# Optimization experiments

Measured on AMD Instinct MI355X. Metric: run time of the kernel, lower is better.

## Reference

```python
import jax, jax.numpy as jnp
import numpy as np

B, N, E, C = 2, 10000, 150000, 256
EPS = 1e-5  # torch BatchNorm1d default eps


def _bn(x, gamma, beta):
    # BatchNorm1d in training mode: biased batch statistics over the row dim.
    m = x.mean(axis=0)
    v = x.var(axis=0)
    return (x - m) * jax.lax.rsqrt(v + EPS) * gamma + beta


def setup_inputs() -> dict:
    key = jax.random.key(0)
    ks = jax.random.split(key, 6)
    xyz = jax.random.normal(ks[0], (B, N, 3), jnp.float32)
    features = jax.random.normal(ks[1], (B, C, N), jnp.float32)
    edges = jax.random.randint(ks[2], (B, 2, E), 0, N, jnp.int32)
    W_e = jax.random.normal(ks[3], (C + 3, C), jnp.float32) * 0.02
    b_e = jnp.zeros((C,), jnp.float32)
    g_e = jnp.ones((C,), jnp.float32)
    beta_e = jnp.zeros((C,), jnp.float32)
    W_u = jax.random.normal(ks[4], (C, C), jnp.float32) * 0.02
    b_u = jnp.zeros((C,), jnp.float32)
    g_u = jnp.ones((C,), jnp.float32)
    beta_u = jnp.zeros((C,), jnp.float32)
    return {"xyz": xyz, "features": features, "edges": edges,
            "W_e": W_e, "b_e": b_e, "g_e": g_e, "beta_e": beta_e,
            "W_u": W_u, "b_u": b_u, "g_u": g_u, "beta_u": beta_u}


def reference(xyz, features, edges, W_e, b_e, g_e, beta_e, W_u, b_u, g_u, beta_u):
    vf = jnp.transpose(features, (0, 2, 1))        # [B, N, C]
    ed = jnp.transpose(edges, (0, 2, 1))           # [B, E, 2]
    src, dst = ed[..., 0], ed[..., 1]              # [B, E]
    gather = jax.vmap(lambda v, i: v[i])
    s_feat = gather(vf, src)                       # [B, E, C]
    s_xyz = gather(xyz, src)                       # [B, E, 3]
    d_xyz = gather(xyz, dst)                       # [B, E, 3]
    ef = jnp.concatenate([s_feat, s_xyz - d_xyz], axis=-1).reshape(-1, C + 3)
    h = _bn(jax.nn.relu(ef @ W_e + b_e), g_e, beta_e).reshape(B, E, C)
    # scatter-max by destination vertex
    agg = jax.vmap(lambda f, i: jax.ops.segment_max(f, i, num_segments=N))(h, dst)
    agg = jnp.where(jnp.isfinite(agg), agg, 0.0)   # empty segments -> 0 (torch_scatter fill)
    u = _bn(jax.nn.relu(agg.reshape(-1, C) @ W_u + b_u), g_u, beta_u).reshape(B, N, C)
    out = u + vf                                   # residual
    return jnp.transpose(out, (0, 2, 1))           # [B, C, N]
```

## Files before the change

### kernel.cpp

```cpp
#include <hip/hip_runtime.h>

#define B_ 2
#define N_ 10000
#define E_ 150000
#define C_ 256
#define M_EDGE (B_*E_)
#define M_NODE (B_*N_)
#define ED_CAP (M_EDGE + 3*M_NODE + 64)
#define NW_ 4096
#define SPAN_CAP 256
#define EPS_ 1e-5f

typedef unsigned short u16;
typedef unsigned int   u32;
typedef unsigned long long u64;
typedef __attribute__((ext_vector_type(8))) __bf16 bf16x8;
typedef __attribute__((ext_vector_type(4))) float  f32x4;
typedef _Float16 h2 __attribute__((ext_vector_type(2)));

__device__ __forceinline__ u16 f2bf(float x) {
  union { float f; u32 u; } v; v.f = x;
  u32 r = v.u + 0x7FFFu + ((v.u >> 16) & 1u);
  return (u16)(r >> 16);
}
__device__ __forceinline__ float bf2f(u16 x) {
  union { u32 u; float f; } v; v.u = ((u32)x) << 16; return v.f;
}
__device__ __forceinline__ u16 f2h(float x) {
  _Float16 h = (_Float16)x;
  union { _Float16 h; u16 u; } v; v.h = h; return v.u;
}
__device__ __forceinline__ float h2f(u32 bits) {
  union { u16 u; _Float16 h; } v; v.u = (u16)bits; return (float)v.h;
}
__device__ __forceinline__ h2 u2h2(u32 x) {
  union { u32 u; h2 h; } v; v.u = x; return v.h;
}
__device__ __forceinline__ u32 h22u(h2 x) {
  union { h2 h; u32 u; } v; v.h = x; return v.u;
}

__device__ __forceinline__ void async16(void* lds, const void* g) {
  __builtin_amdgcn_global_load_lds(
      (const __attribute__((address_space(1))) void*)g,
      (__attribute__((address_space(3))) void*)lds, 16, 0, 0);
}

__device__ __forceinline__ u32 zload(const u16* zp, u32 si) {
  u32 r;
  u64 a = (u64)(zp + ((size_t)si << 8));
  asm volatile("global_load_dword %0, %1, off" : "=v"(r) : "v"(a) : "memory");
  return r;
}

__global__ void k_transpose_feat(const float* __restrict__ f, u16* __restrict__ vf,
                                 int* __restrict__ counts, float* __restrict__ stats) {
  __shared__ float tile[32][33];
  int tx = threadIdx.x & 31, ty = threadIdx.x >> 5;
  int b = blockIdx.z, c0 = blockIdx.y * 32, n0 = blockIdx.x * 32;
  if (blockIdx.y == 0 && blockIdx.z == 0) {
    int i = blockIdx.x * 256 + threadIdx.x;
    if (i < M_NODE) counts[i] = 0;
    if (i < 1024) stats[i] = 0.f;
  }
  #pragma unroll
  for (int i = 0; i < 4; i++) {
    int c = c0 + ty + i*8, n = n0 + tx;
    tile[ty + i*8][tx] = (n < N_) ? f[((size_t)(b*C_ + c))*N_ + n] : 0.f;
  }
  __syncthreads();
  #pragma unroll
  for (int i = 0; i < 4; i++) {
    int n = n0 + ty + i*8, c = c0 + tx;
    if (n < N_) vf[((size_t)(b*N_ + n))*C_ + c] = f2bf(tile[tx][ty + i*8]);
  }
}

__global__ void k_transpose_w(const float* __restrict__ We, const float* __restrict__ Wu,
                              u16* __restrict__ WeT, u16* __restrict__ WuT) {
  __shared__ float tile[32][33];
  const float* src = blockIdx.z ? Wu : We;
  u16* dst = blockIdx.z ? WuT : WeT;
  int tx = threadIdx.x & 31, ty = threadIdx.x >> 5;
  int r0 = blockIdx.y * 32, c0 = blockIdx.x * 32;
  #pragma unroll
  for (int i = 0; i < 4; i++)
    tile[ty + i*8][tx] = src[(size_t)(r0 + ty + i*8)*C_ + c0 + tx];
  __syncthreads();
  #pragma unroll
  for (int i = 0; i < 4; i++)
    dst[(size_t)(c0 + ty + i*8)*C_ + r0 + tx] = f2bf(tile[tx][ty + i*8]);
}

__global__ void k_hist(const int* __restrict__ edges, int* __restrict__ counts) {
  int i = blockIdx.x * 256 + threadIdx.x;
  if (i >= M_EDGE) return;
  int b = (i >= E_) ? 1 : 0;
  int e = i - b * E_;
  int d = edges[(size_t)(b*2 + 1)*E_ + e];
  atomicAdd(&counts[b*N_ + d], 1);
}

__global__ __launch_bounds__(1024)
void k_scan(const int* __restrict__ counts, int* __restrict__ offs, int* __restrict__ cursor) {
  __shared__ int wsum[16];
  int t = threadIdx.x;
  int lane = t & 63, wv = t >> 6;
  int base = t * 20;
  int vals[20];
  if (t < 1000) {
    #pragma unroll
    for (int j = 0; j < 5; j++)
      *(int4*)&vals[j*4] = *(const int4*)&counts[base + j*4];
  } else {
    #pragma unroll
    for (int i = 0; i < 20; i++) vals[i] = 0;
  }
  int local[20];
  int tot = 0;
  #pragma unroll
  for (int i = 0; i < 20; i++) {
    int pv = (vals[i] + 3) & ~3;
    local[i] = tot; tot += pv;
  }
  int inc = tot;
  #pragma unroll
  for (int d = 1; d < 64; d <<= 1) {
    int v = __shfl_up(inc, d, 64);
    if (lane >= d) inc += v;
  }
  if (lane == 63) wsum[wv] = inc;
  __syncthreads();
  if (t < 16) {
    int v = wsum[t];
    int inc2 = v;
    #pragma unroll
    for (int d = 1; d < 16; d <<= 1) {
      int x = __shfl_up(inc2, d, 16);
      if (t >= d) inc2 += x;
    }
    wsum[t] = inc2 - v;
  }
  __syncthreads();
  int excl = wsum[wv] + inc - tot;
  if (t < 1000) {
    #pragma unroll
    for (int j = 0; j < 5; j++) {
      int4 o;
      o.x = excl + local[j*4 + 0];
      o.y = excl + local[j*4 + 1];
      o.z = excl + local[j*4 + 2];
      o.w = excl + local[j*4 + 3];
      *(int4*)&offs[base + j*4]   = o;
      *(int4*)&cursor[base + j*4] = o;
    }
  }
  if (t == 1023) offs[M_NODE] = excl + tot;
}

__global__ void k_scatter(const int* __restrict__ edges, const float* __restrict__ xyz,
                          int* __restrict__ cursor, uint2* __restrict__ ed) {
  int i = blockIdx.x * 256 + threadIdx.x;
  if (i >= M_EDGE) return;
  int b = (i >= E_) ? 1 : 0;
  int e = i - b * E_;
  int s = edges[(size_t)(b*2 + 0)*E_ + e];
  int d = edges[(size_t)(b*2 + 1)*E_ + e];
  const float* ps = xyz + ((size_t)(b*N_ + s))*3;
  const float* pd = xyz + ((size_t)(b*N_ + d))*3;
  int pos = atomicAdd(&cursor[b*N_ + d], 1);
  u32 rx = (u32)f2h(ps[0]-pd[0]) | ((u32)f2h(ps[1]-pd[1]) << 16);
  u32 ry = (u32)f2h(ps[2]-pd[2]) | ((u32)(b*N_ + s) << 16);
  ed[pos] = make_uint2(rx, ry);
}

__global__ void k_pad(const int* __restrict__ offs, const int* __restrict__ counts,
                      uint2* __restrict__ ed, u32* __restrict__ nodeInfo,
                      int* __restrict__ waveStart) {
  int i = blockIdx.x * 256 + threadIdx.x;
  const int T = offs[M_NODE];
  const int SPW = (T + NW_ - 1) / NW_;
  if (i < M_NODE) {
    int s = offs[i], e = offs[i+1];
    int cnt = counts[i];
    if (cnt > 0) {
      int pad = e - (s + cnt);
      if (pad) {
        uint2 f = ed[s];
        for (int k = 0; k < pad; k++) ed[s + cnt + k] = f;
      }
    }
    nodeInfo[i] = ((u32)e << 10) | (u32)cnt;
    int lo = (i == 0) ? 0 : offs[i-1] + 1;
    int wlo = (lo + SPW - 1) / SPW;
    int whi = offs[i] / SPW;
    for (int w = wlo; w <= whi && w <= NW_; w++) waveStart[w] = i;
  }
  if (i == M_NODE) {
    nodeInfo[M_NODE]   = ((u32)T << 10);
    nodeInfo[M_NODE+1] = ((u32)T << 10);
    int lo = offs[M_NODE-1] + 1;
    int wlo = (lo + SPW - 1) / SPW;
    if (wlo < 0) wlo = 0;
    for (int w = wlo; w <= NW_; w++) waveStart[w] = M_NODE;
  }
  int pos = T + i;
  if (pos < ED_CAP) ed[pos] = make_uint2(0u, 0u);
}

__global__ __launch_bounds__(256)
void k_zgemm(const u16* __restrict__ A, const u16* __restrict__ WeT,
             const float* __restrict__ be, u16* __restrict__ zh)
{
  __shared__ __align__(16) u16 As[128*32];
  __shared__ __align__(16) u16 Bs[128*32];
  const int t  = threadIdx.x;
  const int n0 = blockIdx.x * 128;
  const int mb = blockIdx.y * 128;

  int r0 = mb + (t >> 2);      if (r0 >= M_NODE) r0 = 0;
  int r1 = mb + 64 + (t >> 2); if (r1 >= M_NODE) r1 = 0;
  const int ak = (((t & 3) ^ ((t >> 3) & 3)) << 3);
  const u16* asrc0 = A + (size_t)r0 * C_ + ak;
  const u16* asrc1 = A + (size_t)r1 * C_ + ak;
  const u16* bsrc0 = WeT + (size_t)(n0 + (t >> 2)) * C_ + ak;
  const u16* bsrc1 = WeT + (size_t)(n0 + 64 + (t >> 2)) * C_ + ak;

  const f32x4 zero = {0.f, 0.f, 0.f, 0.f};
  f32x4 acc[4][4];
  #pragma unroll
  for (int m = 0; m < 4; m++)
    #pragma unroll
    for (int n = 0; n < 4; n++) acc[m][n] = zero;

  const int lane = t & 63, wave = t >> 6;
  const int wr = wave >> 1, wc = wave & 1;
  const int lr = lane & 15, lch = lane >> 4;
  const int swz = (lr >> 1) & 3;

  for (int kk = 0; kk < 8; kk++) {
    const int k0 = kk * 32;
    async16(&As[t*8],        asrc0 + k0);
    async16(&As[(t+256)*8],  asrc1 + k0);
    async16(&Bs[t*8],        bsrc0 + k0);
    async16(&Bs[(t+256)*8],  bsrc1 + k0);
    __syncthreads();
    bf16x8 a[4], b[4];
    #pragma unroll
    for (int m = 0; m < 4; m++)
      a[m] = *(const bf16x8*)&As[(wr*64 + m*16 + lr)*32 + ((lch ^ swz) << 3)];
    #pragma unroll
    for (int n = 0; n < 4; n++)
      b[n] = *(const bf16x8*)&Bs[(wc*64 + n*16 + lr)*32 + ((lch ^ swz) << 3)];
    #pragma unroll
    for (int m = 0; m < 4; m++)
      #pragma unroll
      for (int n = 0; n < 4; n++)
        acc[m][n] = __builtin_amdgcn_mfma_f32_16x16x32_bf16(a[m], b[n], acc[m][n], 0, 0, 0);
    __syncthreads();
  }

  int gc[4]; float bias[4];
  #pragma unroll
  for (int n = 0; n < 4; n++) { int c = n0 + wc*64 + n*16 + lr; gc[n] = c; bias[n] = be[c]; }
  #pragma unroll
  for (int m = 0; m < 4; m++) {
    #pragma unroll
    for (int j = 0; j < 4; j++) {
      int r = mb + wr*64 + m*16 + lch*4 + j;
      if (r < M_NODE) {
        #pragma unroll
        for (int n = 0; n < 4; n++)
          zh[(size_t)r * C_ + gc[n]] = f2h(acc[m][n][j] + bias[n]);
      }
    }
  }
}

__global__ __launch_bounds__(512)
void k_agg(const u16* __restrict__ zh, const uint2* __restrict__ ed,
           const int* __restrict__ offs, const u32* __restrict__ nodeInfo,
           const int* __restrict__ waveStart,
           const float* __restrict__ We, const float* __restrict__ ge,
           u32* __restrict__ aggh, float* __restrict__ esum, float* __restrict__ esumsq)
{
  __shared__ __align__(16) uint2 rec[8][SPAN_CAP];
  __shared__ float red[8][128];

  const int tid  = threadIdx.x;
  const int lane = tid & 63;
  const int wave = __builtin_amdgcn_readfirstlane(tid >> 6);
  const int grp  = __builtin_amdgcn_readfirstlane(blockIdx.x & 1);
  const int c0   = grp * 128 + lane * 2;
  const h2 w0 = h2{(_Float16)We[256*C_ + c0], (_Float16)We[256*C_ + c0 + 1]};
  const h2 w1 = h2{(_Float16)We[257*C_ + c0], (_Float16)We[257*C_ + c0 + 1]};
  const h2 w2 = h2{(_Float16)We[258*C_ + c0], (_Float16)We[258*C_ + c0 + 1]};
  const float ge0 = ge[c0], ge1 = ge[c0 + 1];
  const u16* zp = zh + c0;

  const h2 hzero = h2{(_Float16)0.f, (_Float16)0.f};
  const h2 MXI = h2{(_Float16)-1.f, (_Float16)-1.f};
  const h2 MNI = h2{(_Float16)65504.f, (_Float16)65504.f};
  h2 psh = hzero, pqh = hzero;

  const int wid  = (blockIdx.x >> 1) * 8 + wave;
  int cur        = __builtin_amdgcn_readfirstlane(waveStart[wid]);
  const int nEnd = __builtin_amdgcn_readfirstlane(waveStart[wid + 1]);

  if (cur < nEnd) {
    const int uBeg = __builtin_amdgcn_readfirstlane(offs[cur]);
    const int uEnd = __builtin_amdgcn_readfirstlane(offs[nEnd]);
    const int span = uEnd - uBeg;
    if (span > 0) {
      for (int s = lane; s < span; s += 64) rec[wave][s] = ed[uBeg + s];

      u32 info = nodeInfo[cur];
      while ((int)(info >> 10) == uBeg) { cur++; info = nodeInfo[cur]; }
      int curEnd   = (int)(info >> 10);
      int vE       = uBeg + (int)(info & 1023u);
      u32 nextInfo = nodeInfo[cur + 1];

      h2 mx = MXI, mn = MNI;
      const int nc = span >> 2;
      u32 Z[8][4];

      auto flushNode = [&]() {
        h2 s;
        s.x = (ge0 >= 0.f) ? mx.x : mn.x;
        s.y = (ge1 >= 0.f) ? mx.y : mn.y;
        aggh[(size_t)cur * 128 + grp * 64 + lane] = h22u(s);
      };

#define ISSUEZ(ZB, CI) { \
      int _c = (CI) < nc - 1 ? (CI) : nc - 1; \
      uint4 _a = *(const uint4*)&rec[wave][_c*4]; \
      uint4 _b = *(const uint4*)&rec[wave][_c*4 + 2]; \
      Z[ZB][0] = zload(zp, _a.y >> 16); \
      Z[ZB][1] = zload(zp, _a.w >> 16); \
      Z[ZB][2] = zload(zp, _b.y >> 16); \
      Z[ZB][3] = zload(zp, _b.w >> 16); }

#define PROCSLOT(RX, RY, ZV, KOFF) { \
      h2 dxx = u2h2(((RX) & 0xffffu) | ((RX) << 16)); \
      h2 dyy = u2h2(((RX) >> 16) | ((RX) & 0xffff0000u)); \
      h2 dzz = u2h2(((RY) & 0xffffu) | ((RY) << 16)); \
      h2 y = dxx*w0 + dyy*w1 + dzz*w2 + u2h2(ZV); \
      y = __builtin_elementwise_max(y, hzero); \
      mx = __builtin_elementwise_max(mx, y); \
      mn = __builtin_elementwise_min(mn, y); \
      if (slot + (KOFF) < vE) { psh = psh + y; pqh = y*y + pqh; } }

#define PHASE(J, ZW, ZR) { \
      uint4 rA = *(const uint4*)&rec[wave][(J)*4]; \
      uint4 rB = *(const uint4*)&rec[wave][(J)*4 + 2]; \
      ISSUEZ(ZW, (J) + 5) \
      asm volatile("s_waitcnt vmcnt(20)" ::: "memory"); \
      __builtin_amdgcn_sched_barrier(0); \
      const int slot = uBeg + (J)*4; \
      if (slot == curEnd) { \
        flushNode(); \
        mx = MXI; mn = MNI; \
        cur++; \
        u32 inf = nextInfo; \
        while ((int)(inf >> 10) == curEnd) { cur++; inf = nodeInfo[cur]; } \
        vE = curEnd + (int)(inf & 1023u); \
        curEnd = (int)(inf >> 10); \
        nextInfo = nodeInfo[cur + 1]; \
      } \
      PROCSLOT(rA.x, rA.y, Z[ZR][0], 0) \
      PROCSLOT(rA.z, rA.w, Z[ZR][1], 1) \
      PROCSLOT(rB.x, rB.y, Z[ZR][2], 2) \
      PROCSLOT(rB.z, rB.w, Z[ZR][3], 3) }

      ISSUEZ(0, 0) ISSUEZ(1, 1) ISSUEZ(2, 2) ISSUEZ(3, 3) ISSUEZ(4, 4)

      for (int j = 0; j < nc; j += 8) {
        PHASE(j + 0, 5, 0)
        if (j + 1 < nc) PHASE(j + 1, 6, 1)
        if (j + 2 < nc) PHASE(j + 2, 7, 2)
        if (j + 3 < nc) PHASE(j + 3, 0, 3)
        if (j + 4 < nc) PHASE(j + 4, 1, 4)
        if (j + 5 < nc) PHASE(j + 5, 2, 5)
        if (j + 6 < nc) PHASE(j + 6, 3, 6)
        if (j + 7 < nc) PHASE(j + 7, 4, 7)
      }
      flushNode();
#undef ISSUEZ
#undef PROCSLOT
#undef PHASE
    }
  }

  float ps0 = (float)psh.x, ps1 = (float)psh.y;
  float pq0 = (float)pqh.x, pq1 = (float)pqh.y;
  red[wave][lane*2]     = ps0;
  red[wave][lane*2 + 1] = ps1;
  __syncthreads();
  if (tid < 128) {
    float s = 0.f;
    #pragma unroll
    for (int w = 0; w < 8; w++) s += red[w][tid];
    atomicAdd(&esum[grp*128 + tid], s);
  }
  __syncthreads();
  red[wave][lane*2]     = pq0;
  red[wave][lane*2 + 1] = pq1;
  __syncthreads();
  if (tid < 128) {
    float s = 0.f;
    #pragma unroll
    for (int w = 0; w < 8; w++) s += red[w][tid];
    atomicAdd(&esumsq[grp*128 + tid], s);
  }
}

__global__ __launch_bounds__(256)
void k_ugemm(const u32* __restrict__ aggh, const int* __restrict__ counts,
             const float* __restrict__ esum, const float* __restrict__ esumsq,
             const float* __restrict__ ge, const float* __restrict__ bte,
             const u16* __restrict__ WuT, const float* __restrict__ bu,
             u16* __restrict__ yu, float* __restrict__ usum, float* __restrict__ usumsq)
{
  __shared__ __align__(16) u16 As[128*32];
  __shared__ __align__(16) u16 Bs[128*32];
  __shared__ float sscale[256], sshift[256];
  const int t  = threadIdx.x;
  const int n0 = blockIdx.x * 128;
  const int mb = blockIdx.y * 128;

  {
    float m = esum[t] / (float)M_EDGE;
    float v = esumsq[t] / (float)M_EDGE - m*m;
    v = fmaxf(v, 0.f);
    float s = ge[t] * rsqrtf(v + EPS_);
    sscale[t] = s;
    sshift[t] = bte[t] - m*s;
  }

  int r0 = mb + (t >> 2);      if (r0 >= M_NODE) r0 = 0;
  int r1 = mb + 64 + (t >> 2); if (r1 >= M_NODE) r1 = 0;
  const int ak = (((t & 3) ^ ((t >> 3) & 3)) << 3);
  const bool nz0 = counts[r0] > 0;
  const bool nz1 = counts[r1] > 0;
  const u32* ag0 = aggh + (size_t)r0 * 128 + (ak >> 1);
  const u32* ag1 = aggh + (size_t)r1 * 128 + (ak >> 1);
  const u16* bsrc0 = WuT + (size_t)(n0 + (t >> 2)) * C_ + ak;
  const u16* bsrc1 = WuT + (size_t)(n0 + 64 + (t >> 2)) * C_ + ak;

  const f32x4 zero = {0.f, 0.f, 0.f, 0.f};
  f32x4 acc[4][4];
  #pragma unroll
  for (int m = 0; m < 4; m++)
    #pragma unroll
    for (int n = 0; n < 4; n++) acc[m][n] = zero;

  const int lane = t & 63, wave = t >> 6;
  const int wr = wave >> 1, wc = wave & 1;
  const int lr = lane & 15, lch = lane >> 4;
  const int swz = (lr >> 1) & 3;

  __syncthreads();

  for (int kk = 0; kk < 8; kk++) {
    const int k0 = kk * 32;
    uint4 a0 = *(const uint4*)(ag0 + (k0 >> 1));
    uint4 a1 = *(const uint4*)(ag1 + (k0 >> 1));
    const int base = k0 + ak;
    float4 sc0 = *(const float4*)&sscale[base];
    float4 sc1 = *(const float4*)&sscale[base + 4];
    float4 sh0 = *(const float4*)&sshift[base];
    float4 sh1 = *(const float4*)&sshift[base + 4];
    auto cvt = [&](u32 q, float s0, float b0, float s1, float b1, bool nz) -> u32 {
      float v0 = nz ? fmaf(h2f(q & 0xffffu), s0, b0) : 0.f;
      float v1 = nz ? fmaf(h2f(q >> 16),     s1, b1) : 0.f;
      return ((u32)f2bf(v0)) | (((u32)f2bf(v1)) << 16);
    };
    uint4 p0, p1;
    p0.x = cvt(a0.x, sc0.x, sh0.x, sc0.y, sh0.y, nz0);
    p0.y = cvt(a0.y, sc0.z, sh0.z, sc0.w, sh0.w, nz0);
    p0.z = cvt(a0.z, sc1.x, sh1.x, sc1.y, sh1.y, nz0);
    p0.w = cvt(a0.w, sc1.z, sh1.z, sc1.w, sh1.w, nz0);
    p1.x = cvt(a1.x, sc0.x, sh0.x, sc0.y, sh0.y, nz1);
    p1.y = cvt(a1.y, sc0.z, sh0.z, sc0.w, sh0.w, nz1);
    p1.z = cvt(a1.z, sc1.x, sh1.x, sc1.y, sh1.y, nz1);
    p1.w = cvt(a1.w, sc1.z, sh1.z, sc1.w, sh1.w, nz1);
    *(uint4*)&As[t*8]       = p0;
    *(uint4*)&As[(t+256)*8] = p1;
    async16(&Bs[t*8],        bsrc0 + k0);
    async16(&Bs[(t+256)*8],  bsrc1 + k0);
    __syncthreads();
    bf16x8 a[4], b[4];
    #pragma unroll
    for (int m = 0; m < 4; m++)
      a[m] = *(const bf16x8*)&As[(wr*64 + m*16 + lr)*32 + ((lch ^ swz) << 3)];
    #pragma unroll
    for (int n = 0; n < 4; n++)
      b[n] = *(const bf16x8*)&Bs[(wc*64 + n*16 + lr)*32 + ((lch ^ swz) << 3)];
    #pragma unroll
    for (int m = 0; m < 4; m++)
      #pragma unroll
      for (int n = 0; n < 4; n++)
        acc[m][n] = __builtin_amdgcn_mfma_f32_16x16x32_bf16(a[m], b[n], acc[m][n], 0, 0, 0);
    __syncthreads();
  }

  int gc[4]; float bias[4];
  #pragma unroll
  for (int n = 0; n < 4; n++) { int c = n0 + wc*64 + n*16 + lr; gc[n] = c; bias[n] = bu[c]; }
  float psum[4] = {0.f,0.f,0.f,0.f};
  float psq [4] = {0.f,0.f,0.f,0.f};
  #pragma unroll
  for (int m = 0; m < 4; m++) {
    #pragma unroll
    for (int j = 0; j < 4; j++) {
      int r = mb + wr*64 + m*16 + lch*4 + j;
      bool valid = r < M_NODE;
      #pragma unroll
      for (int n = 0; n < 4; n++) {
        float y = fmaxf(acc[m][n][j] + bias[n], 0.f);
        if (valid) {
          psum[n] += y;
          psq[n]  += y*y;
          yu[(size_t)r * C_ + gc[n]] = f2bf(y);
        }
      }
    }
  }
  #pragma unroll
  for (int n = 0; n < 4; n++) {
    float s1 = psum[n], s2 = psq[n];
    s1 += __shfl_xor(s1, 16, 64);  s2 += __shfl_xor(s2, 16, 64);
    s1 += __shfl_xor(s1, 32, 64);  s2 += __shfl_xor(s2, 32, 64);
    if (lch == 0) { atomicAdd(&usum[gc[n]], s1); atomicAdd(&usumsq[gc[n]], s2); }
  }
}

__global__ void k_final(const u16* __restrict__ yu, const u16* __restrict__ vf,
                        const float* __restrict__ usum, const float* __restrict__ usumsq,
                        const float* __restrict__ gu, const float* __restrict__ btu,
                        float* __restrict__ out) {
  __shared__ float tile[32][33];
  __shared__ float sc[32], sh[32];
  int tx = threadIdx.x & 31, ty = threadIdx.x >> 5;
  int b = blockIdx.z, c0 = blockIdx.y * 32, n0 = blockIdx.x * 32;
  if (threadIdx.x < 32) {
    int c = c0 + threadIdx.x;
    float m = usum[c] / (float)M_NODE;
    float v = usumsq[c] / (float)M_NODE - m*m;
    v = fmaxf(v, 0.f);
    float s = gu[c] * rsqrtf(v + EPS_);
    sc[threadIdx.x] = s;
    sh[threadIdx.x] = btu[c] - m*s;
  }
  __syncthreads();
  #pragma unroll
  for (int i = 0; i < 4; i++) {
    int n = n0 + ty + i*8, c = c0 + tx;
    float v = 0.f;
    if (n < N_) {
      size_t idx = ((size_t)(b*N_ + n))*C_ + c;
      v = bf2f(yu[idx]) * sc[tx] + sh[tx] + bf2f(vf[idx]);
    }
    tile[ty + i*8][tx] = v;
  }
  __syncthreads();
  int n = n0 + tx;
  if (n < N_) {
    #pragma unroll
    for (int i = 0; i < 4; i++) {
      int c = c0 + ty + i*8;
      out[((size_t)(b*C_ + c))*N_ + n] = tile[tx][ty + i*8];
    }
  }
}

extern "C" void kernel_launch(void* const* d_in, const int* in_sizes, int n_in,
                              void* d_out, int out_size, void* d_ws, size_t ws_size,
                              hipStream_t stream) {
  const float* xyz  = (const float*)d_in[0];
  const float* feat = (const float*)d_in[1];
  const int*   edges= (const int*)  d_in[2];
  const float* We   = (const float*)d_in[3];
  const float* be   = (const float*)d_in[4];
  const float* ge   = (const float*)d_in[5];
  const float* bte  = (const float*)d_in[6];
  const float* Wu   = (const float*)d_in[7];
  const float* bu   = (const float*)d_in[8];
  const float* gu   = (const float*)d_in[9];
  const float* btu  = (const float*)d_in[10];
  float* out = (float*)d_out;

  char* w = (char*)d_ws;
  size_t off = 0;
  auto carve = [&](size_t bytes) -> void* {
    void* p = w + off;
    off = (off + bytes + 511) & ~(size_t)511;
    return p;
  };
  u16*  vf       = (u16*) carve((size_t)M_NODE*C_*2);
  u16*  WeT      = (u16*) carve((size_t)C_*C_*2);
  u16*  WuT      = (u16*) carve((size_t)C_*C_*2);
  u16*  zh       = (u16*) carve((size_t)M_NODE*C_*2);
  uint2* ed      = (uint2*)carve((size_t)ED_CAP*8);
  int*  counts   = (int*) carve((size_t)M_NODE*4);
  int*  offs     = (int*) carve((size_t)(M_NODE+1)*4);
  int*  cursor   = (int*) carve((size_t)M_NODE*4);
  u32*  nodeInfo = (u32*) carve((size_t)(M_NODE+2)*4);
  int*  waveStart= (int*) carve((size_t)(NW_+1)*4);
  u32*  aggh     = (u32*) carve((size_t)M_NODE*128*4);
  u16*  yu       = (u16*) carve((size_t)M_NODE*C_*2);
  float* stats   = (float*)carve(2048*4);
  float* esum = stats,        *esumsq = stats + 256;
  float* usum = stats + 512,  *usumsq = stats + 768;

  k_transpose_feat<<<dim3((N_+31)/32, C_/32, B_), 256, 0, stream>>>(feat, vf, counts, stats);
  k_transpose_w<<<dim3(C_/32, C_/32, 2), 256, 0, stream>>>(We, Wu, WeT, WuT);
  k_hist<<<dim3((M_EDGE + 255)/256), 256, 0, stream>>>(edges, counts);
  k_scan<<<1, 1024, 0, stream>>>(counts, offs, cursor);
  k_scatter<<<dim3((M_EDGE + 255)/256), 256, 0, stream>>>(edges, xyz, cursor, ed);
  k_pad<<<dim3((M_NODE + 255)/256), 256, 0, stream>>>(offs, counts, ed, nodeInfo, waveStart);
  k_zgemm<<<dim3(2, (M_NODE + 127)/128), 256, 0, stream>>>(vf, WeT, be, zh);
  k_agg<<<dim3(NW_/8*2), 512, 0, stream>>>(zh, ed, offs, nodeInfo, waveStart,
                                           We, ge, aggh, esum, esumsq);
  k_ugemm<<<dim3(2, (M_NODE + 127)/128), 256, 0, stream>>>(
      aggh, counts, esum, esumsq, ge, bte, WuT, bu, yu, usum, usumsq);
  k_final<<<dim3((N_+31)/32, C_/32, B_), 256, 0, stream>>>(
      yu, vf, usum, usumsq, gu, btu, out);
}
```

Baseline: 142.4 us.

## Fuse graph-build kernels into one cooperative kernel and merge weight transpose

The separate histogram, scan, scatter and pad kernels become one cooperative kernel that separates phases with grid-wide syncs. The scan is rewritten for a 512-thread block, with each thread covering 40 counts. The weight transpose moves into an extra z-slice of the feature transpose launch. The goal is to cut kernel launch overhead and the gaps between small dependent kernels. In exchange, the scan phase runs on a single block while the rest of the grid waits at a barrier, and the grid-sync barriers have their own cost.

```diff
diff --git a/kernel.cpp b/kernel.cpp
--- a/kernel.cpp
+++ b/kernel.cpp
@@ -1,4 +1,7 @@
 #include <hip/hip_runtime.h>
+#include <hip/hip_cooperative_groups.h>
+
+namespace cg = cooperative_groups;
 
 #define B_ 2
 #define N_ 10000
@@ -54,9 +57,27 @@
 }
 
 __global__ void k_transpose_feat(const float* __restrict__ f, u16* __restrict__ vf,
+                                 const float* __restrict__ We, const float* __restrict__ Wu,
+                                 u16* __restrict__ WeT, u16* __restrict__ WuT,
                                  int* __restrict__ counts, float* __restrict__ stats) {
   __shared__ float tile[32][33];
   int tx = threadIdx.x & 31, ty = threadIdx.x >> 5;
+  if (blockIdx.z == 2) {
+    if (blockIdx.y != 0 || blockIdx.x >= 128) return;
+    int idx = blockIdx.x;
+    const float* src = (idx >= 64) ? Wu : We;
+    u16* dst = (idx >= 64) ? WuT : WeT;
+    int rem = idx & 63;
+    int r0 = (rem >> 3) * 32, c0 = (rem & 7) * 32;
+    #pragma unroll
+    for (int i = 0; i < 4; i++)
+      tile[ty + i*8][tx] = src[(size_t)(r0 + ty + i*8)*C_ + c0 + tx];
+    __syncthreads();
+    #pragma unroll
+    for (int i = 0; i < 4; i++)
+      dst[(size_t)(c0 + ty + i*8)*C_ + r0 + tx] = f2bf(tile[tx][ty + i*8]);
+    return;
+  }
   int b = blockIdx.z, c0 = blockIdx.y * 32, n0 = blockIdx.x * 32;
   if (blockIdx.y == 0 && blockIdx.z == 0) {
     int i = blockIdx.x * 256 + threadIdx.x;
@@ -76,136 +97,123 @@
   }
 }
 
-__global__ void k_transpose_w(const float* __restrict__ We, const float* __restrict__ Wu,
-                              u16* __restrict__ WeT, u16* __restrict__ WuT) {
-  __shared__ float tile[32][33];
-  const float* src = blockIdx.z ? Wu : We;
-  u16* dst = blockIdx.z ? WuT : WeT;
-  int tx = threadIdx.x & 31, ty = threadIdx.x >> 5;
-  int r0 = blockIdx.y * 32, c0 = blockIdx.x * 32;
-  #pragma unroll
-  for (int i = 0; i < 4; i++)
-    tile[ty + i*8][tx] = src[(size_t)(r0 + ty + i*8)*C_ + c0 + tx];
-  __syncthreads();
-  #pragma unroll
-  for (int i = 0; i < 4; i++)
-    dst[(size_t)(c0 + ty + i*8)*C_ + r0 + tx] = f2bf(tile[tx][ty + i*8]);
-}
-
-__global__ void k_hist(const int* __restrict__ edges, int* __restrict__ counts) {
-  int i = blockIdx.x * 256 + threadIdx.x;
-  if (i >= M_EDGE) return;
-  int b = (i >= E_) ? 1 : 0;
-  int e = i - b * E_;
-  int d = edges[(size_t)(b*2 + 1)*E_ + e];
-  atomicAdd(&counts[b*N_ + d], 1);
-}
-
-__global__ __launch_bounds__(1024)
-void k_scan(const int* __restrict__ counts, int* __restrict__ offs, int* __restrict__ cursor) {
-  __shared__ int wsum[16];
-  int t = threadIdx.x;
-  int lane = t & 63, wv = t >> 6;
-  int base = t * 20;
-  int vals[20];
-  if (t < 1000) {
-    #pragma unroll
-    for (int j = 0; j < 5; j++)
-      *(int4*)&vals[j*4] = *(const int4*)&counts[base + j*4];
-  } else {
-    #pragma unroll
-    for (int i = 0; i < 20; i++) vals[i] = 0;
-  }
-  int local[20];
-  int tot = 0;
-  #pragma unroll
-  for (int i = 0; i < 20; i++) {
-    int pv = (vals[i] + 3) & ~3;
-    local[i] = tot; tot += pv;
-  }
-  int inc = tot;
-  #pragma unroll
-  for (int d = 1; d < 64; d <<= 1) {
-    int v = __shfl_up(inc, d, 64);
-    if (lane >= d) inc += v;
-  }
-  if (lane == 63) wsum[wv] = inc;
-  __syncthreads();
-  if (t < 16) {
-    int v = wsum[t];
-    int inc2 = v;
-    #pragma unroll
-    for (int d = 1; d < 16; d <<= 1) {
-      int x = __shfl_up(inc2, d, 16);
-      if (t >= d) inc2 += x;
-    }
-    wsum[t] = inc2 - v;
-  }
-  __syncthreads();
-  int excl = wsum[wv] + inc - tot;
-  if (t < 1000) {
-    #pragma unroll
-    for (int j = 0; j < 5; j++) {
-      int4 o;
-      o.x = excl + local[j*4 + 0];
-      o.y = excl + local[j*4 + 1];
-      o.z = excl + local[j*4 + 2];
-      o.w = excl + local[j*4 + 3];
-      *(int4*)&offs[base + j*4]   = o;
-      *(int4*)&cursor[base + j*4] = o;
-    }
-  }
-  if (t == 1023) offs[M_NODE] = excl + tot;
-}
-
-__global__ void k_scatter(const int* __restrict__ edges, const float* __restrict__ xyz,
-                          int* __restrict__ cursor, uint2* __restrict__ ed) {
-  int i = blockIdx.x * 256 + threadIdx.x;
-  if (i >= M_EDGE) return;
-  int b = (i >= E_) ? 1 : 0;
-  int e = i - b * E_;
-  int s = edges[(size_t)(b*2 + 0)*E_ + e];
-  int d = edges[(size_t)(b*2 + 1)*E_ + e];
-  const float* ps = xyz + ((size_t)(b*N_ + s))*3;
-  const float* pd = xyz + ((size_t)(b*N_ + d))*3;
-  int pos = atomicAdd(&cursor[b*N_ + d], 1);
-  u32 rx = (u32)f2h(ps[0]-pd[0]) | ((u32)f2h(ps[1]-pd[1]) << 16);
-  u32 ry = (u32)f2h(ps[2]-pd[2]) | ((u32)(b*N_ + s) << 16);
-  ed[pos] = make_uint2(rx, ry);
-}
-
-__global__ void k_pad(const int* __restrict__ offs, const int* __restrict__ counts,
-                      uint2* __restrict__ ed, u32* __restrict__ nodeInfo,
-                      int* __restrict__ waveStart) {
-  int i = blockIdx.x * 256 + threadIdx.x;
+__global__ __launch_bounds__(512)
+void k_graph(const int* __restrict__ edges, const float* __restrict__ xyz,
+             int* __restrict__ counts, int* __restrict__ offs, int* __restrict__ cursor,
+             uint2* __restrict__ ed, u32* __restrict__ nodeInfo,
+             int* __restrict__ waveStart)
+{
+  cg::grid_group grid = cg::this_grid();
+  const int tid = threadIdx.x;
+  const int gsz = gridDim.x * 512;
+  const int gid = blockIdx.x * 512 + tid;
+
+  for (int i = gid; i < M_EDGE; i += gsz) {
+    int b = (i >= E_) ? 1 : 0;
+    int e = i - b * E_;
+    int d = edges[(size_t)(b*2 + 1)*E_ + e];
+    atomicAdd(&counts[b*N_ + d], 1);
+  }
+  grid.sync();
+
+  if (blockIdx.x == 0) {
+    __shared__ int wsum[8];
+    int lane = tid & 63, wv = tid >> 6;
+    int base = tid * 40;
+    int local[40];
+    int tot = 0;
+    if (tid < 500) {
+      #pragma unroll
+      for (int j = 0; j < 10; j++) {
+        int4 v = *(const int4*)&counts[base + j*4];
+        int p0 = (v.x + 3) & ~3, p1 = (v.y + 3) & ~3;
+        int p2 = (v.z + 3) & ~3, p3 = (v.w + 3) & ~3;
+        local[j*4+0] = tot; tot += p0;
+        local[j*4+1] = tot; tot += p1;
+        local[j*4+2] = tot; tot += p2;
+        local[j*4+3] = tot; tot += p3;
+      }
+    }
+    int inc = tot;
+    #pragma unroll
+    for (int d = 1; d < 64; d <<= 1) {
+      int v = __shfl_up(inc, d, 64);
+      if (lane >= d) inc += v;
+    }
+    if (lane == 63) wsum[wv] = inc;
+    __syncthreads();
+    if (tid < 8) {
+      int v = wsum[tid];
+      int s = v;
+      #pragma unroll
+      for (int d = 1; d < 8; d <<= 1) {
+        int x = __shfl_up(s, d, 64);
+        if (tid >= d) s += x;
+      }
+      wsum[tid] = s - v;
+    }
+    __syncthreads();
+    int excl = wsum[wv] + inc - tot;
+    if (tid < 500) {
+      #pragma unroll
+      for (int j = 0; j < 10; j++) {
+        int4 o;
+        o.x = excl + local[j*4+0];
+        o.y = excl + local[j*4+1];
+        o.z = excl + local[j*4+2];
+        o.w = excl + local[j*4+3];
+        *(int4*)&offs[base + j*4]   = o;
+        *(int4*)&cursor[base + j*4] = o;
+      }
+    }
+    if (tid == 511) offs[M_NODE] = excl;
+  }
+  grid.sync();
+
+  for (int i = gid; i < M_EDGE; i += gsz) {
+    int b = (i >= E_) ? 1 : 0;
+    int e = i - b * E_;
+    int s = edges[(size_t)(b*2 + 0)*E_ + e];
+    int d = edges[(size_t)(b*2 + 1)*E_ + e];
+    const float* ps = xyz + ((size_t)(b*N_ + s))*3;
+    const float* pd = xyz + ((size_t)(b*N_ + d))*3;
+    int pos = atomicAdd(&cursor[b*N_ + d], 1);
+    u32 rx = (u32)f2h(ps[0]-pd[0]) | ((u32)f2h(ps[1]-pd[1]) << 16);
+    u32 ry = (u32)f2h(ps[2]-pd[2]) | ((u32)(b*N_ + s) << 16);
+    ed[pos] = make_uint2(rx, ry);
+  }
+  grid.sync();
+
   const int T = offs[M_NODE];
   const int SPW = (T + NW_ - 1) / NW_;
-  if (i < M_NODE) {
-    int s = offs[i], e = offs[i+1];
+  for (int i = gid; i < M_NODE; i += gsz) {
+    int s = offs[i], e2 = offs[i+1];
     int cnt = counts[i];
     if (cnt > 0) {
-      int pad = e - (s + cnt);
+      int pad = e2 - (s + cnt);
       if (pad) {
         uint2 f = ed[s];
         for (int k = 0; k < pad; k++) ed[s + cnt + k] = f;
       }
     }
-    nodeInfo[i] = ((u32)e << 10) | (u32)cnt;
+    nodeInfo[i] = ((u32)e2 << 10) | (u32)cnt;
     int lo = (i == 0) ? 0 : offs[i-1] + 1;
     int wlo = (lo + SPW - 1) / SPW;
     int whi = offs[i] / SPW;
-    for (int w = wlo; w <= whi && w <= NW_; w++) waveStart[w] = i;
-  }
-  if (i == M_NODE) {
+    for (int w2 = wlo; w2 <= whi && w2 <= NW_; w2++) waveStart[w2] = i;
+  }
+  if (gid == 0) {
     nodeInfo[M_NODE]   = ((u32)T << 10);
     nodeInfo[M_NODE+1] = ((u32)T << 10);
     int lo = offs[M_NODE-1] + 1;
     int wlo = (lo + SPW - 1) / SPW;
     if (wlo < 0) wlo = 0;
-    for (int w = wlo; w <= NW_; w++) waveStart[w] = M_NODE;
-  }
-  int pos = T + i;
-  if (pos < ED_CAP) ed[pos] = make_uint2(0u, 0u);
+    for (int w2 = wlo; w2 <= NW_; w2++) waveStart[w2] = M_NODE;
+  }
+  {
+    int pos = T + gid;
+    if (pos < ED_CAP) ed[pos] = make_uint2(0u, 0u);
+  }
 }
 
 __global__ __launch_bounds__(256)
@@ -613,12 +621,14 @@
   float* esum = stats,        *esumsq = stats + 256;
   float* usum = stats + 512,  *usumsq = stats + 768;
 
-  k_transpose_feat<<<dim3((N_+31)/32, C_/32, B_), 256, 0, stream>>>(feat, vf, counts, stats);
-  k_transpose_w<<<dim3(C_/32, C_/32, 2), 256, 0, stream>>>(We, Wu, WeT, WuT);
-  k_hist<<<dim3((M_EDGE + 255)/256), 256, 0, stream>>>(edges, counts);
-  k_scan<<<1, 1024, 0, stream>>>(counts, offs, cursor);
-  k_scatter<<<dim3((M_EDGE + 255)/256), 256, 0, stream>>>(edges, xyz, cursor, ed);
-  k_pad<<<dim3((M_NODE + 255)/256), 256, 0, stream>>>(offs, counts, ed, nodeInfo, waveStart);
+  k_transpose_feat<<<dim3((N_+31)/32, C_/32, 3), 256, 0, stream>>>(
+      feat, vf, We, Wu, WeT, WuT, counts, stats);
+  {
+    void* args[] = { (void*)&edges, (void*)&xyz, (void*)&counts, (void*)&offs,
+                     (void*)&cursor, (void*)&ed, (void*)&nodeInfo, (void*)&waveStart };
+    hipLaunchCooperativeKernel((const void*)k_graph, dim3(320), dim3(512),
+                               args, 0, stream);
+  }
   k_zgemm<<<dim3(2, (M_NODE + 127)/128), 256, 0, stream>>>(vf, WeT, be, zh);
   k_agg<<<dim3(NW_/8*2), 512, 0, stream>>>(zh, ed, offs, nodeInfo, waveStart,
                                            We, ge, aggh, esum, esumsq);
```

New measurement: 267.2 us. 1.88x slower.
